# Kernel optimization log

Measured on AMD Instinct MI355X. Metric: run time of the kernel, lower is better.

## Reference

```python
import jax, jax.numpy as jnp
import numpy as np

N_NODES = 100000
N_EDGES = 1600000
D = 64
N_LAYERS = 3


def setup_inputs() -> dict:
    key = jax.random.key(0)
    k1, k2, k3, k4 = jax.random.split(key, 4)
    x = jax.random.normal(k1, (N_NODES, D), dtype=jnp.float32)
    edge_index = jax.random.randint(k2, (2, N_EDGES), 0, N_NODES, dtype=jnp.int64)
    scale = 1.0 / np.sqrt(D)
    Wl = jax.random.normal(k3, (N_LAYERS, D, D), dtype=jnp.float32) * scale
    Wr = jax.random.normal(k4, (N_LAYERS, D, D), dtype=jnp.float32) * scale
    b = jnp.zeros((N_LAYERS, D), dtype=jnp.float32)
    return {"x": x, "edge_index": edge_index, "Wl": Wl, "Wr": Wr, "b": b}


def _sage_conv(x, src, dst, Wl, Wr, b, n_nodes):
    # mean-aggregate source features onto targets, then two linear maps
    msgs = x[src]                                              # [E, d]
    summed = jax.ops.segment_sum(msgs, dst, num_segments=n_nodes)   # [N, d]
    cnt = jax.ops.segment_sum(jnp.ones(src.shape[0], x.dtype), dst,
                              num_segments=n_nodes)            # [N]
    agg = summed / jnp.maximum(cnt, 1.0)[:, None]
    return agg @ Wl + x @ Wr + b


def reference(x, edge_index, Wl, Wr, b):
    # GraphSAGE forward in eval mode (dropout is identity, p=0.5 only in training)
    src, dst = edge_index[0], edge_index[1]
    n = x.shape[0]
    h = x
    for i in range(N_LAYERS - 1):
        h = _sage_conv(h, src, dst, Wl[i], Wr[i], b[i], n)
        h = jax.nn.relu(h)
    h = _sage_conv(h, src, dst, Wl[-1], Wr[-1], b[-1], n)
    return h
```

## Files before the change

### kernel.cpp

```cpp
#include <hip/hip_runtime.h>
#include <hip/hip_fp16.h>

#define DD 64
#define NPB 32
#define EPC 8192
#define BK_SHIFT 8
#define BNODES 256
#define SCHUNK 1024
#define APAD 136

typedef _Float16 half8 __attribute__((ext_vector_type(8)));
typedef float f32x4 __attribute__((ext_vector_type(4)));

union U8 { uint2 u; __half2 h[2]; };

__global__ __launch_bounds__(256) void f32_to_f16_kernel(const float* __restrict__ in,
                                                         __half* __restrict__ out, int n8) {
    int i = blockIdx.x * blockDim.x + threadIdx.x;
    if (i < n8) {
        const float4* p = reinterpret_cast<const float4*>(in + (size_t)i * 8);
        float4 a = p[0], b = p[1];
        __half2* q = reinterpret_cast<__half2*>(out + (size_t)i * 8);
        q[0] = __floats2half2_rn(a.x, a.y);
        q[1] = __floats2half2_rn(a.z, a.w);
        q[2] = __floats2half2_rn(b.x, b.y);
        q[3] = __floats2half2_rn(b.z, b.w);
    }
}

__global__ __launch_bounds__(256) void wswz_kernel(const float* __restrict__ Wl,
                                                   const float* __restrict__ Wr,
                                                   __half* __restrict__ Wswz, int nlayer) {
    int idx = blockIdx.x * 256 + threadIdx.x;
    int total = nlayer * 4 * 4 * 64;
    if (idx >= total) return;
    int lane = idx & 63;
    int nt   = (idx >> 6) & 3;
    int kt   = (idx >> 8) & 3;
    int L    = idx >> 10;
    int n     = nt * 16 + (lane & 15);
    int kbase = kt * 32 + 8 * (lane >> 4);
    __half* o = Wswz + (size_t)idx * 8;
#pragma unroll
    for (int i = 0; i < 8; ++i) {
        int k = kbase + i;
        float v = (k < 64) ? Wl[(size_t)L * 4096 + (size_t)k * 64 + n]
                           : Wr[(size_t)L * 4096 + (size_t)(k - 64) * 64 + n];
        o[i] = __float2half(v);
    }
}

__global__ __launch_bounds__(256) void binA_kernel(const int* __restrict__ dst, int e, int nc,
                                                   int* __restrict__ histT, int nbuck) {
    __shared__ int h[512];
    int tid = threadIdx.x, c = blockIdx.x;
    for (int i = tid; i < nbuck; i += 256) h[i] = 0;
    __syncthreads();
    int base = c * EPC;
#pragma unroll
    for (int j = 0; j < EPC / 256; ++j) {
        int i = base + j * 256 + tid;
        if (i < e) atomicAdd(&h[dst[i] >> BK_SHIFT], 1);
    }
    __syncthreads();
    for (int b = tid; b < nbuck; b += 256) histT[b * nc + c] = h[b];
}

__global__ __launch_bounds__(256) void scan_part_kernel(const int* __restrict__ data, int tot,
                                                        int* __restrict__ blocksum) {
    __shared__ int red[256];
    int tid = threadIdx.x;
    int base = blockIdx.x * SCHUNK + tid * 4;
    int s = 0;
#pragma unroll
    for (int j = 0; j < 4; ++j) {
        int i = base + j;
        if (i < tot) s += data[i];
    }
    red[tid] = s;
    __syncthreads();
    for (int off = 128; off > 0; off >>= 1) {
        if (tid < off) red[tid] += red[tid + off];
        __syncthreads();
    }
    if (tid == 0) blocksum[blockIdx.x] = red[0];
}

__global__ __launch_bounds__(1024) void scan_mid_kernel(int* __restrict__ blocksum, int nb) {
    __shared__ int sc[1024];
    int tid = threadIdx.x;
    int v = (tid < nb) ? blocksum[tid] : 0;
    sc[tid] = v;
    __syncthreads();
    for (int off = 1; off < 1024; off <<= 1) {
        int t = (tid >= off) ? sc[tid - off] : 0;
        __syncthreads();
        sc[tid] += t;
        __syncthreads();
    }
    if (tid < nb) blocksum[tid] = sc[tid] - v;
}

__global__ __launch_bounds__(256) void scan_write_kernel(int* __restrict__ data, int tot,
                                                         const int* __restrict__ blockoff) {
    __shared__ int sc[256];
    int tid = threadIdx.x;
    int base = blockIdx.x * SCHUNK + tid * 4;
    int e0 = 0, e1 = 0, e2 = 0, e3 = 0;
    if (base + 0 < tot) e0 = data[base + 0];
    if (base + 1 < tot) e1 = data[base + 1];
    if (base + 2 < tot) e2 = data[base + 2];
    if (base + 3 < tot) e3 = data[base + 3];
    int s = e0 + e1 + e2 + e3;
    sc[tid] = s;
    __syncthreads();
    for (int off = 1; off < 256; off <<= 1) {
        int t = (tid >= off) ? sc[tid - off] : 0;
        __syncthreads();
        sc[tid] += t;
        __syncthreads();
    }
    int run = blockoff[blockIdx.x] + sc[tid] - s;
    if (base + 0 < tot) data[base + 0] = run;
    if (base + 1 < tot) data[base + 1] = run + e0;
    if (base + 2 < tot) data[base + 2] = run + e0 + e1;
    if (base + 3 < tot) data[base + 3] = run + e0 + e1 + e2;
}

__global__ __launch_bounds__(256) void binB_kernel(const int* __restrict__ src, const int* __restrict__ dst,
                                                   int e, int nc, const int* __restrict__ offT,
                                                   int nbuck, int* __restrict__ binned) {
    __shared__ int cur[512];
    int tid = threadIdx.x, c = blockIdx.x;
    for (int b = tid; b < nbuck; b += 256) cur[b] = offT[b * nc + c];
    __syncthreads();
    int base = c * EPC;
#pragma unroll
    for (int j = 0; j < EPC / 256; ++j) {
        int i = base + j * 256 + tid;
        if (i < e) {
            int d = dst[i];
            int p = atomicAdd(&cur[d >> BK_SHIFT], 1);
            binned[p] = (unsigned)(d & (BNODES - 1)) << 24 | (unsigned)src[i];
        }
    }
}

__global__ __launch_bounds__(BNODES) void place_kernel(const int* __restrict__ binned,
                                                       const int* __restrict__ offT, int nc,
                                                       int nbuck, int e, int n,
                                                       int* __restrict__ rowp, int* __restrict__ esrc) {
    __shared__ int deg[BNODES];
    __shared__ int sc[BNODES];
    int tid = threadIdx.x, b = blockIdx.x;
    int node0 = b << BK_SHIFT;
    int base = offT[b * nc];
    int end  = (b + 1 < nbuck) ? offT[(b + 1) * nc] : e;
    deg[tid] = 0;
    __syncthreads();
    for (int i = base + tid; i < end; i += BNODES)
        atomicAdd(&deg[(unsigned)binned[i] >> 24], 1);
    __syncthreads();
    int v = deg[tid];
    sc[tid] = v;
    __syncthreads();
    for (int off = 1; off < BNODES; off <<= 1) {
        int t = (tid >= off) ? sc[tid - off] : 0;
        __syncthreads();
        sc[tid] += t;
        __syncthreads();
    }
    int excl = sc[tid] - v;
    int node = node0 + tid;
    if (node < n) rowp[node] = base + excl;
    if (b == 0 && tid == 0) rowp[n] = e;
    deg[tid] = base + excl;
    __syncthreads();
    for (int i = base + tid; i < end; i += BNODES) {
        int p = binned[i];
        int pos = atomicAdd(&deg[(unsigned)p >> 24], 1);
        esrc[pos] = p & 0xFFFFFF;
    }
}

__global__ __launch_bounds__(512) void sage_layer_kernel(
    const __half* __restrict__ hin16, const float* __restrict__ self32,
    const int* __restrict__ rowp, const int* __restrict__ esrc,
    const __half* __restrict__ Bfrag,
    const float* __restrict__ bias,
    float* __restrict__ out32, __half* __restrict__ out16,
    int n, int relu)
{
    __shared__ _Float16 sA[NPB][APAD];

    int tid = threadIdx.x;
    int grp = tid >> 4;
    int l   = tid & 15;
    int node = blockIdx.x * NPB + grp;

    if (node < n) {
        if (self32) {
            float4 h4 = *reinterpret_cast<const float4*>(self32 + (size_t)node * DD + l * 4);
            U8 pk; pk.h[0] = __floats2half2_rn(h4.x, h4.y); pk.h[1] = __floats2half2_rn(h4.z, h4.w);
            *reinterpret_cast<uint2*>(&sA[grp][64 + 4 * l]) = pk.u;
        } else {
            uint2 v = *reinterpret_cast<const uint2*>(hin16 + (size_t)node * DD + l * 4);
            *reinterpret_cast<uint2*>(&sA[grp][64 + 4 * l]) = v;
        }

        int beg = rowp[node], end = rowp[node + 1];
        float ax = 0.f, ay = 0.f, az = 0.f, aw = 0.f;
        int t = beg;
        for (; t + 4 <= end; t += 4) {
            int s0 = esrc[t + 0], s1 = esrc[t + 1], s2 = esrc[t + 2], s3 = esrc[t + 3];
            U8 v0, v1, v2, v3;
            v0.u = *reinterpret_cast<const uint2*>(hin16 + (size_t)s0 * DD + l * 4);
            v1.u = *reinterpret_cast<const uint2*>(hin16 + (size_t)s1 * DD + l * 4);
            v2.u = *reinterpret_cast<const uint2*>(hin16 + (size_t)s2 * DD + l * 4);
            v3.u = *reinterpret_cast<const uint2*>(hin16 + (size_t)s3 * DD + l * 4);
            float2 a0 = __half22float2(v0.h[0]), b0 = __half22float2(v0.h[1]);
            float2 a1 = __half22float2(v1.h[0]), b1 = __half22float2(v1.h[1]);
            float2 a2 = __half22float2(v2.h[0]), b2 = __half22float2(v2.h[1]);
            float2 a3 = __half22float2(v3.h[0]), b3 = __half22float2(v3.h[1]);
            ax += (a0.x + a1.x) + (a2.x + a3.x);
            ay += (a0.y + a1.y) + (a2.y + a3.y);
            az += (b0.x + b1.x) + (b2.x + b3.x);
            aw += (b0.y + b1.y) + (b2.y + b3.y);
        }
        for (; t < end; ++t) {
            int s = esrc[t];
            U8 v; v.u = *reinterpret_cast<const uint2*>(hin16 + (size_t)s * DD + l * 4);
            float2 f0 = __half22float2(v.h[0]), f1 = __half22float2(v.h[1]);
            ax += f0.x; ay += f0.y; az += f1.x; aw += f1.y;
        }
        float inv = 1.0f / fmaxf((float)(end - beg), 1.0f);
        U8 pk; pk.h[0] = __floats2half2_rn(ax * inv, ay * inv);
               pk.h[1] = __floats2half2_rn(az * inv, aw * inv);
        *reinterpret_cast<uint2*>(&sA[grp][4 * l]) = pk.u;
    }
    __syncthreads();

    int wave  = tid >> 6;
    int lane  = tid & 63;
    int mtile = wave >> 2;
    int nt    = wave & 3;
    int arow  = mtile * 16 + (lane & 15);
    f32x4 acc = {0.f, 0.f, 0.f, 0.f};
    const half8* bfr = reinterpret_cast<const half8*>(Bfrag);
#pragma unroll
    for (int kt = 0; kt < 4; ++kt) {
        half8 a = *reinterpret_cast<const half8*>(&sA[arow][kt * 32 + 8 * (lane >> 4)]);
        half8 b = bfr[(kt * 4 + nt) * 64 + lane];
        acc = __builtin_amdgcn_mfma_f32_16x16x32_f16(a, b, acc, 0, 0, 0);
    }
    int col = nt * 16 + (lane & 15);
    float bv = bias[col];
    int rbase = blockIdx.x * NPB + mtile * 16 + (lane >> 4) * 4;
#pragma unroll
    for (int j = 0; j < 4; ++j) {
        int r = rbase + j;
        if (r < n) {
            float o = acc[j] + bv;
            if (relu) o = fmaxf(o, 0.f);
            if (out32) out32[(size_t)r * DD + col] = o;
            if (out16) out16[(size_t)r * DD + col] = __float2half(o);
        }
    }
}

extern "C" void kernel_launch(void* const* d_in, const int* in_sizes, int n_in,
                              void* d_out, int out_size, void* d_ws, size_t ws_size,
                              hipStream_t stream) {
    (void)n_in; (void)out_size; (void)ws_size;
    const float* x  = (const float*)d_in[0];
    const int*   ei = (const int*)d_in[1];
    const float* Wl = (const float*)d_in[2];
    const float* Wr = (const float*)d_in[3];
    const float* bb = (const float*)d_in[4];
    float* out = (float*)d_out;

    int n = in_sizes[0] / DD;
    int e = in_sizes[1] / 2;
    const int* src = ei;
    const int* dst = ei + e;

    int nc    = (e + EPC - 1) / EPC;
    int nbuck = (n + BNODES - 1) >> BK_SHIFT;
    int tot   = nbuck * nc;
    int nsb   = (tot + SCHUNK - 1) / SCHUNK;

    char* cur = (char*)d_ws;
    auto alloc = [&](size_t bytes) -> void* {
        void* p = (void*)cur;
        cur += (bytes + 255) & ~(size_t)255;
        return p;
    };
    int*    histT  = (int*)alloc((size_t)tot * 4);
    int*    bsum   = (int*)alloc(1024 * 4);
    int*    binned = (int*)alloc((size_t)e * 4);
    int*    rowp   = (int*)alloc(((size_t)n + 1) * 4);
    int*    esrc   = (int*)alloc((size_t)e * 4);
    __half* x16    = (__half*)alloc((size_t)n * DD * 2);
    __half* hA16   = (__half*)alloc((size_t)n * DD * 2);
    __half* hB16   = (__half*)alloc((size_t)n * DD * 2);
    __half* Wswz   = (__half*)alloc((size_t)3 * 8192 * 2);

    int n8 = n * DD / 8;
    f32_to_f16_kernel<<<(n8 + 255) / 256, 256, 0, stream>>>(x, x16, n8);
    wswz_kernel<<<(3 * 4 * 4 * 64 + 255) / 256, 256, 0, stream>>>(Wl, Wr, Wswz, 3);

    binA_kernel<<<nc, 256, 0, stream>>>(dst, e, nc, histT, nbuck);
    scan_part_kernel<<<nsb, 256, 0, stream>>>(histT, tot, bsum);
    scan_mid_kernel<<<1, 1024, 0, stream>>>(bsum, nsb);
    scan_write_kernel<<<nsb, 256, 0, stream>>>(histT, tot, bsum);
    binB_kernel<<<nc, 256, 0, stream>>>(src, dst, e, nc, histT, nbuck, binned);
    place_kernel<<<nbuck, BNODES, 0, stream>>>(binned, histT, nc, nbuck, e, n, rowp, esrc);

    int lb = (n + NPB - 1) / NPB;
    sage_layer_kernel<<<lb, 512, 0, stream>>>(x16,  x,       rowp, esrc, Wswz,         bb,          nullptr, hA16, n, 1);
    sage_layer_kernel<<<lb, 512, 0, stream>>>(hA16, nullptr, rowp, esrc, Wswz + 8192,  bb + DD,     nullptr, hB16, n, 1);
    sage_layer_kernel<<<lb, 512, 0, stream>>>(hB16, nullptr, rowp, esrc, Wswz + 16384, bb + 2 * DD, out,     nullptr, n, 0);
}
```

Measured before the change: 199.7 us.

## Gather 16-byte rows with 8 lanes per node, 64 nodes per block

The aggregation phase now uses 8 threads per node, each loading 16 bytes (8 halves), instead of 16 threads loading 8 bytes. This doubles the nodes per 512-thread block to 64. The edge loop is unrolled by 8 with a 4-edge tail to keep more gathers in flight. In the MFMA stage each wave preloads its B fragments once and reuses them across two M tiles. The aim is fewer, wider memory transactions and more memory-level parallelism in the gather. The cost is higher register pressure and fewer blocks in the grid.

```diff
diff --git a/kernel.cpp b/kernel.cpp
--- a/kernel.cpp
+++ b/kernel.cpp
@@ -2,7 +2,7 @@
 #include <hip/hip_fp16.h>
 
 #define DD 64
-#define NPB 32
+#define NPB 64
 #define EPC 8192
 #define BK_SHIFT 8
 #define BNODES 256
@@ -12,7 +12,8 @@
 typedef _Float16 half8 __attribute__((ext_vector_type(8)));
 typedef float f32x4 __attribute__((ext_vector_type(4)));
 
-union U8 { uint2 u; __half2 h[2]; };
+union U8  { uint2 u; __half2 h[2]; };
+union U16 { uint4 u; __half2 h[4]; };
 
 __global__ __launch_bounds__(256) void f32_to_f16_kernel(const float* __restrict__ in,
                                                          __half* __restrict__ out, int n8) {
@@ -194,76 +195,103 @@
     __shared__ _Float16 sA[NPB][APAD];
 
     int tid = threadIdx.x;
-    int grp = tid >> 4;
-    int l   = tid & 15;
+    int grp = tid >> 3;
+    int l   = tid & 7;
     int node = blockIdx.x * NPB + grp;
 
     if (node < n) {
         if (self32) {
-            float4 h4 = *reinterpret_cast<const float4*>(self32 + (size_t)node * DD + l * 4);
-            U8 pk; pk.h[0] = __floats2half2_rn(h4.x, h4.y); pk.h[1] = __floats2half2_rn(h4.z, h4.w);
-            *reinterpret_cast<uint2*>(&sA[grp][64 + 4 * l]) = pk.u;
+            const float4* p = reinterpret_cast<const float4*>(self32 + (size_t)node * DD + l * 8);
+            float4 a = p[0], b = p[1];
+            U16 pk;
+            pk.h[0] = __floats2half2_rn(a.x, a.y);
+            pk.h[1] = __floats2half2_rn(a.z, a.w);
+            pk.h[2] = __floats2half2_rn(b.x, b.y);
+            pk.h[3] = __floats2half2_rn(b.z, b.w);
+            *reinterpret_cast<uint4*>(&sA[grp][64 + 8 * l]) = pk.u;
         } else {
-            uint2 v = *reinterpret_cast<const uint2*>(hin16 + (size_t)node * DD + l * 4);
-            *reinterpret_cast<uint2*>(&sA[grp][64 + 4 * l]) = v;
+            uint4 v = *reinterpret_cast<const uint4*>(hin16 + (size_t)node * DD + l * 8);
+            *reinterpret_cast<uint4*>(&sA[grp][64 + 8 * l]) = v;
         }
 
         int beg = rowp[node], end = rowp[node + 1];
-        float ax = 0.f, ay = 0.f, az = 0.f, aw = 0.f;
+        float a0 = 0, a1 = 0, a2 = 0, a3 = 0, a4 = 0, a5 = 0, a6 = 0, a7 = 0;
+#define ACC8(V) { float2 f0 = __half22float2(V.h[0]), f1 = __half22float2(V.h[1]); \
+                  float2 f2 = __half22float2(V.h[2]), f3 = __half22float2(V.h[3]); \
+                  a0 += f0.x; a1 += f0.y; a2 += f1.x; a3 += f1.y; \
+                  a4 += f2.x; a5 += f2.y; a6 += f3.x; a7 += f3.y; }
         int t = beg;
-        for (; t + 4 <= end; t += 4) {
+        for (; t + 8 <= end; t += 8) {
             int s0 = esrc[t + 0], s1 = esrc[t + 1], s2 = esrc[t + 2], s3 = esrc[t + 3];
-            U8 v0, v1, v2, v3;
-            v0.u = *reinterpret_cast<const uint2*>(hin16 + (size_t)s0 * DD + l * 4);
-            v1.u = *reinterpret_cast<const uint2*>(hin16 + (size_t)s1 * DD + l * 4);
-            v2.u = *reinterpret_cast<const uint2*>(hin16 + (size_t)s2 * DD + l * 4);
-            v3.u = *reinterpret_cast<const uint2*>(hin16 + (size_t)s3 * DD + l * 4);
-            float2 a0 = __half22float2(v0.h[0]), b0 = __half22float2(v0.h[1]);
-            float2 a1 = __half22float2(v1.h[0]), b1 = __half22float2(v1.h[1]);
-            float2 a2 = __half22float2(v2.h[0]), b2 = __half22float2(v2.h[1]);
-            float2 a3 = __half22float2(v3.h[0]), b3 = __half22float2(v3.h[1]);
-            ax += (a0.x + a1.x) + (a2.x + a3.x);
-            ay += (a0.y + a1.y) + (a2.y + a3.y);
-            az += (b0.x + b1.x) + (b2.x + b3.x);
-            aw += (b0.y + b1.y) + (b2.y + b3.y);
+            int s4 = esrc[t + 4], s5 = esrc[t + 5], s6 = esrc[t + 6], s7 = esrc[t + 7];
+            U16 v0, v1, v2, v3, v4, v5, v6, v7;
+            v0.u = *reinterpret_cast<const uint4*>(hin16 + (size_t)s0 * DD + l * 8);
+            v1.u = *reinterpret_cast<const uint4*>(hin16 + (size_t)s1 * DD + l * 8);
+            v2.u = *reinterpret_cast<const uint4*>(hin16 + (size_t)s2 * DD + l * 8);
+            v3.u = *reinterpret_cast<const uint4*>(hin16 + (size_t)s3 * DD + l * 8);
+            v4.u = *reinterpret_cast<const uint4*>(hin16 + (size_t)s4 * DD + l * 8);
+            v5.u = *reinterpret_cast<const uint4*>(hin16 + (size_t)s5 * DD + l * 8);
+            v6.u = *reinterpret_cast<const uint4*>(hin16 + (size_t)s6 * DD + l * 8);
+            v7.u = *reinterpret_cast<const uint4*>(hin16 + (size_t)s7 * DD + l * 8);
+            ACC8(v0); ACC8(v1); ACC8(v2); ACC8(v3);
+            ACC8(v4); ACC8(v5); ACC8(v6); ACC8(v7);
+        }
+        if (t + 4 <= end) {
+            int s0 = esrc[t + 0], s1 = esrc[t + 1], s2 = esrc[t + 2], s3 = esrc[t + 3];
+            U16 v0, v1, v2, v3;
+            v0.u = *reinterpret_cast<const uint4*>(hin16 + (size_t)s0 * DD + l * 8);
+            v1.u = *reinterpret_cast<const uint4*>(hin16 + (size_t)s1 * DD + l * 8);
+            v2.u = *reinterpret_cast<const uint4*>(hin16 + (size_t)s2 * DD + l * 8);
+            v3.u = *reinterpret_cast<const uint4*>(hin16 + (size_t)s3 * DD + l * 8);
+            ACC8(v0); ACC8(v1); ACC8(v2); ACC8(v3);
+            t += 4;
         }
         for (; t < end; ++t) {
             int s = esrc[t];
-            U8 v; v.u = *reinterpret_cast<const uint2*>(hin16 + (size_t)s * DD + l * 4);
-            float2 f0 = __half22float2(v.h[0]), f1 = __half22float2(v.h[1]);
-            ax += f0.x; ay += f0.y; az += f1.x; aw += f1.y;
-        }
+            U16 v; v.u = *reinterpret_cast<const uint4*>(hin16 + (size_t)s * DD + l * 8);
+            ACC8(v);
+        }
+#undef ACC8
         float inv = 1.0f / fmaxf((float)(end - beg), 1.0f);
-        U8 pk; pk.h[0] = __floats2half2_rn(ax * inv, ay * inv);
-               pk.h[1] = __floats2half2_rn(az * inv, aw * inv);
-        *reinterpret_cast<uint2*>(&sA[grp][4 * l]) = pk.u;
-    }
-    __syncthreads();
-
-    int wave  = tid >> 6;
-    int lane  = tid & 63;
-    int mtile = wave >> 2;
-    int nt    = wave & 3;
-    int arow  = mtile * 16 + (lane & 15);
-    f32x4 acc = {0.f, 0.f, 0.f, 0.f};
+        U16 pk;
+        pk.h[0] = __floats2half2_rn(a0 * inv, a1 * inv);
+        pk.h[1] = __floats2half2_rn(a2 * inv, a3 * inv);
+        pk.h[2] = __floats2half2_rn(a4 * inv, a5 * inv);
+        pk.h[3] = __floats2half2_rn(a6 * inv, a7 * inv);
+        *reinterpret_cast<uint4*>(&sA[grp][8 * l]) = pk.u;
+    }
+    __syncthreads();
+
+    int wave = tid >> 6;
+    int lane = tid & 63;
+    int nt   = wave & 3;
+    int mt0  = (wave >> 2) * 2;
     const half8* bfr = reinterpret_cast<const half8*>(Bfrag);
-#pragma unroll
-    for (int kt = 0; kt < 4; ++kt) {
-        half8 a = *reinterpret_cast<const half8*>(&sA[arow][kt * 32 + 8 * (lane >> 4)]);
-        half8 b = bfr[(kt * 4 + nt) * 64 + lane];
-        acc = __builtin_amdgcn_mfma_f32_16x16x32_f16(a, b, acc, 0, 0, 0);
-    }
+    half8 bf[4];
+#pragma unroll
+    for (int kt = 0; kt < 4; ++kt) bf[kt] = bfr[(kt * 4 + nt) * 64 + lane];
     int col = nt * 16 + (lane & 15);
     float bv = bias[col];
-    int rbase = blockIdx.x * NPB + mtile * 16 + (lane >> 4) * 4;
-#pragma unroll
-    for (int j = 0; j < 4; ++j) {
-        int r = rbase + j;
-        if (r < n) {
-            float o = acc[j] + bv;
-            if (relu) o = fmaxf(o, 0.f);
-            if (out32) out32[(size_t)r * DD + col] = o;
-            if (out16) out16[(size_t)r * DD + col] = __float2half(o);
+#pragma unroll
+    for (int i = 0; i < 2; ++i) {
+        int mtile = mt0 + i;
+        int arow  = mtile * 16 + (lane & 15);
+        f32x4 acc = {0.f, 0.f, 0.f, 0.f};
+#pragma unroll
+        for (int kt = 0; kt < 4; ++kt) {
+            half8 a = *reinterpret_cast<const half8*>(&sA[arow][kt * 32 + 8 * (lane >> 4)]);
+            acc = __builtin_amdgcn_mfma_f32_16x16x32_f16(a, bf[kt], acc, 0, 0, 0);
+        }
+        int rbase = blockIdx.x * NPB + mtile * 16 + (lane >> 4) * 4;
+#pragma unroll
+        for (int j = 0; j < 4; ++j) {
+            int r = rbase + j;
+            if (r < n) {
+                float o = acc[j] + bv;
+                if (relu) o = fmaxf(o, 0.f);
+                if (out32) out32[(size_t)r * DD + col] = o;
+                if (out16) out16[(size_t)r * DD + col] = __float2half(o);
+            }
         }
     }
 }
```

New measurement: 201.1 us. About the same (+0.7%).
